# Kernel tuning notes

Measured on AMD Instinct MI355X. Metric: run time of the kernel, lower is better.

## Reference

```python
import jax, jax.numpy as jnp
import numpy as np

P = 16          # patch_size
C = 3           # in_chans
D = 768         # embed_dim
V = 10240       # position_embedding_size
B, H, W = 16, 512, 512
N = (H // P) * (W // P)  # 1024 patches per image


def setup_inputs() -> dict:
    key = jax.random.key(0)
    k1, k2, k3, k4, k5 = jax.random.split(key, 5)
    pixel_values = jax.random.uniform(k1, (B, C, H, W), dtype=jnp.float32)
    position_ids = jax.random.randint(k2, (B, N, 2), 0, 32)  # (x, y) patch coords < pW/pH
    padding_positions = jax.random.randint(k3, (B, N), 0, 2).astype(jnp.bool_)
    w_proj = jax.random.normal(k4, (D, C * P * P), dtype=jnp.float32) * 0.02  # Linear weight (out, in)
    pos_table = jax.random.normal(k5, (2, V, D), dtype=jnp.float32) * 0.02
    return {
        "pixel_values": pixel_values,
        "w_proj": w_proj,
        "pos_table": pos_table,
        "position_ids": position_ids,
        "padding_positions": padding_positions,
    }


def reference(pixel_values, w_proj, pos_table, position_ids, padding_positions):
    b, c, h, w = pixel_values.shape
    ph, pw = h // P, w // P
    # Extract patches in Gemma4 C-P-P flatten order: (B, N, C*P*P)
    x = pixel_values.reshape(b, c, ph, P, pw, P)
    x = jnp.transpose(x, (0, 2, 4, 1, 3, 5)).reshape(b, ph * pw, c * P * P)
    patches = 2.0 * (x - 0.5)
    hidden = jnp.einsum('bnf,df->bnd', patches, w_proj)
    # Position embeddings: one_hot(ids) @ table summed over the 2 axes
    # == direct gather-add: table[0][x_id] + table[1][y_id]
    ids = jnp.clip(position_ids, 0)
    pos = pos_table[0][ids[..., 0]] + pos_table[1][ids[..., 1]]  # (B, N, D)
    pos = jnp.where(padding_positions[..., None], 0.0, pos)
    return hidden + pos
```

## Files before the change

kernel.cpp:

```cpp
#include <hip/hip_runtime.h>
#include <stdint.h>


typedef __attribute__((ext_vector_type(8))) short bfrag_t;
typedef __attribute__((ext_vector_type(4))) float f4_t;
typedef __attribute__((ext_vector_type(8))) unsigned short u16x8;
typedef __attribute__((ext_vector_type(4))) unsigned short u16x4;

#define V_POS 10240

__device__ __forceinline__ unsigned short f2bf(float f) {
    unsigned int u = __float_as_uint(f);
    u += 0x7fffu + ((u >> 16) & 1u);
    return (unsigned short)(u >> 16);
}

__device__ __forceinline__ void async_ld16(const void* g, void* l) {
    __builtin_amdgcn_global_load_lds(
        (const __attribute__((address_space(1))) void*)g,
        (__attribute__((address_space(3))) void*)l, 16, 0, 0);
}

__global__ __launch_bounds__(256) void prep_kernel(
    const float* __restrict__ px, const float* __restrict__ wp,
    unsigned short* __restrict__ A, unsigned short* __restrict__ Wb)
{
    __shared__ unsigned short T[32 * 776];
    int bid = blockIdx.x, tid = threadIdx.x;
    if (bid < 512) {
        int b = bid >> 5, ph = bid & 31;
        const float* pxb = px + ((size_t)b * 3 * 512 + (size_t)ph * 16) * 512;
#pragma unroll 6
        for (int it = 0; it < 24; ++it) {
            int idx = it * 256 + tid;
            int c = idx >> 11, rem = idx & 2047, hl = rem >> 7, w4 = rem & 127;
            float4 v = *(const float4*)(pxb + (size_t)c * 262144 + hl * 512 + (w4 << 2));
            int pw  = w4 >> 2;
            int pxo = (w4 & 3) << 2;
            int k   = c * 256 + hl * 16 + pxo;
            u16x4 o;
            o[0] = f2bf(2.f * v.x - 1.f);
            o[1] = f2bf(2.f * v.y - 1.f);
            o[2] = f2bf(2.f * v.z - 1.f);
            o[3] = f2bf(2.f * v.w - 1.f);
            *(u16x4*)&T[pw * 776 + k] = o;
        }
        __syncthreads();
        int r = tid >> 3, p = tid & 7;
        unsigned short* Arow = A + ((size_t)bid * 32 + r) * 768;
        const unsigned short* Trow = T + r * 776;
#pragma unroll 4
        for (int j = 0; j < 12; ++j) {
            int co = (p + 8 * j) << 3;
            *(u16x8*)(Arow + co) = *(const u16x8*)(Trow + co);
        }
    } else {
        long idx = (long)(bid - 512) * 256 + tid;
        const float4* s = (const float4*)(wp + (idx << 3));
        float4 v0 = s[0], v1 = s[1];
        u16x8 o;
        o[0] = f2bf(v0.x); o[1] = f2bf(v0.y); o[2] = f2bf(v0.z); o[3] = f2bf(v0.w);
        o[4] = f2bf(v1.x); o[5] = f2bf(v1.y); o[6] = f2bf(v1.z); o[7] = f2bf(v1.w);
        *(u16x8*)(Wb + (idx << 3)) = o;
    }
}

__global__ __launch_bounds__(256, 3) void gemm_kernel(
    const unsigned short* __restrict__ A, const unsigned short* __restrict__ Bt,
    const int* __restrict__ pos_ids, const unsigned int* __restrict__ pad_in,
    const float* __restrict__ pos_table, float* __restrict__ out)
{
    __shared__ unsigned short LDS[3 * 8192];

    const int tid  = threadIdx.x;
    const int wave = tid >> 6;
    const int lane = tid & 63;

    const int id   = blockIdx.x;
    const int xcd  = id & 7;
    const int slot = id >> 3;
    const int bmg  = slot / 6;
    const int bm   = xcd * 16 + bmg;
    const int bn   = slot - bmg * 6;
    const int m0   = bm << 7;
    const int n0   = bn << 7;

    const bool u8mode = __any(pad_in[lane] > 1u);

    const int rl = lane >> 2;
    const int g  = (lane & 3) ^ (rl & 3);
    const unsigned short* aga0 = A  + (size_t)(m0 + wave * 32 + rl) * 768 + g * 8;
    const unsigned short* aga1 = aga0 + (size_t)16 * 768;
    const unsigned short* bga0 = Bt + (size_t)(n0 + wave * 32 + rl) * 768 + g * 8;
    const unsigned short* bga1 = bga0 + (size_t)16 * 768;
    const int l0 = wave * 32 * 32;
    const int l1 = l0 + 16 * 32;

    const int fr      = lane & 15;
    const int quad    = lane >> 4;
    const int row_off = (wave & 1) << 6;
    const int col_off = (wave >> 1) << 6;
    const int afro = (row_off + fr) * 32 + ((quad ^ (fr & 3)) << 3);
    const int bfro = (col_off + fr) * 32 + ((quad ^ (fr & 3)) << 3) + 4096;

    f4_t acc[4][4] = {};

    auto issue = [&](int t, int b) {
        unsigned short* Ab = (unsigned short*)LDS + b * 8192;
        unsigned short* Bb = Ab + 4096;
        const int ko = t * 32;
        async_ld16(aga0 + ko, Ab + l0);
        async_ld16(aga1 + ko, Ab + l1);
        async_ld16(bga0 + ko, Bb + l0);
        async_ld16(bga1 + ko, Bb + l1);
    };

    issue(0, 0);
    issue(1, 1);

    int bi = 0;
    for (int t = 0; t < 24; ++t) {
        if (t < 23) __builtin_amdgcn_s_waitcnt(0xF74);
        else        __builtin_amdgcn_s_waitcnt(0xF70);
        __builtin_amdgcn_sched_barrier(0);
        __builtin_amdgcn_s_barrier();
        __builtin_amdgcn_sched_barrier(0);
        if (t < 22) {
            int nb = bi + 2; if (nb >= 3) nb -= 3;
            issue(t + 2, nb);
        }
        const unsigned short* Ar = LDS + bi * 8192 + afro;
        const unsigned short* Br = LDS + bi * 8192 + bfro;
        bfrag_t a[4], b[4];
#pragma unroll
        for (int i = 0; i < 4; ++i) a[i] = *(const bfrag_t*)(Ar + i * 512);
#pragma unroll
        for (int i = 0; i < 4; ++i) b[i] = *(const bfrag_t*)(Br + i * 512);
#pragma unroll
        for (int mi = 0; mi < 4; ++mi)
#pragma unroll
            for (int ni = 0; ni < 4; ++ni)
                acc[mi][ni] = __builtin_amdgcn_mfma_f32_16x16x32_bf16(
                    a[mi], b[ni], acc[mi][ni], 0, 0, 0);
        if (++bi == 3) bi = 0;
    }

    const unsigned char* pad8 = (const unsigned char*)pad_in;
    const int colbase = n0 + col_off;
#pragma unroll
    for (int mi = 0; mi < 4; ++mi) {
#pragma unroll
        for (int reg = 0; reg < 4; ++reg) {
            int gm  = m0 + row_off + mi * 16 + (quad << 2) + reg;
            int xid = pos_ids[2 * gm];
            int yid = pos_ids[2 * gm + 1];
            xid = xid < 0 ? 0 : xid;
            yid = yid < 0 ? 0 : yid;
            bool p = u8mode ? (pad8[gm] != 0) : (pad_in[gm] != 0u);
            const float* t0 = pos_table + (size_t)xid * 768 + colbase;
            const float* t1 = pos_table + (size_t)(V_POS + yid) * 768 + colbase;
            float* orow = out + (size_t)gm * 768 + colbase;
#pragma unroll
            for (int ni = 0; ni < 4; ++ni) {
                int cc = ni * 16 + fr;
                float pos = p ? 0.f : (t0[cc] + t1[cc]);
                orow[cc] = acc[mi][ni][reg] + pos;
            }
        }
    }
}

extern "C" void kernel_launch(void* const* d_in, const int* in_sizes, int n_in,
                              void* d_out, int out_size, void* d_ws, size_t ws_size,
                              hipStream_t stream) {
    const float*        px  = (const float*)d_in[0];
    const float*        wp  = (const float*)d_in[1];
    const float*        pt  = (const float*)d_in[2];
    const int*          pid = (const int*)d_in[3];
    const unsigned int* pad = (const unsigned int*)d_in[4];

    unsigned short* A  = (unsigned short*)d_ws;
    unsigned short* Wb = A + (size_t)16384 * 768;

    prep_kernel<<<800, 256, 0, stream>>>(px, wp, A, Wb);
    gemm_kernel<<<768, 256, 0, stream>>>(A, Wb, pid, pad, pt, (float*)d_out);
}
```

Before: 179.2 us.

## Fuse patch extraction into GEMM and prepack weights into MFMA fragment layout

Removes the intermediate bf16 patch matrix. Each 512-thread block now loads two patch-rows of pixels directly into LDS and converts them to bf16 there, then computes a 64x768 output tile with 32x32x16 MFMAs. Weights are prepacked into a fragment-ordered layout so each wave reads them straight from global/L2 without staging in LDS. This cuts the global write and re-read of A and one kernel's worth of traffic. In exchange it drops the async multi-buffered pipeline, launches only 256 blocks, and relies on cache hits for the repeated weight reads.

```diff
diff --git a/kernel.cpp b/kernel.cpp
--- a/kernel.cpp
+++ b/kernel.cpp
@@ -3,11 +3,12 @@
 
 
 typedef __attribute__((ext_vector_type(8))) short bfrag_t;
-typedef __attribute__((ext_vector_type(4))) float f4_t;
+typedef __attribute__((ext_vector_type(16))) float f16acc;
 typedef __attribute__((ext_vector_type(8))) unsigned short u16x8;
 typedef __attribute__((ext_vector_type(4))) unsigned short u16x4;
 
 #define V_POS 10240
+#define RSA 776
 
 __device__ __forceinline__ unsigned short f2bf(float f) {
     unsigned int u = __float_as_uint(f);
@@ -15,156 +16,106 @@
     return (unsigned short)(u >> 16);
 }
 
-__device__ __forceinline__ void async_ld16(const void* g, void* l) {
-    __builtin_amdgcn_global_load_lds(
-        (const __attribute__((address_space(1))) void*)g,
-        (__attribute__((address_space(3))) void*)l, 16, 0, 0);
+__global__ __launch_bounds__(256) void bpack_kernel(
+    const float* __restrict__ wp, unsigned short* __restrict__ Bp)
+{
+    int u     = blockIdx.x * 256 + threadIdx.x;
+    int chunk = u >> 6;
+    int lane  = u & 63;
+    int n32   = chunk / 48;
+    int k16   = chunk - n32 * 48;
+    int n     = (n32 << 5) + (lane & 31);
+    int k     = (k16 << 4) + ((lane >> 5) << 3);
+    const float* s = wp + (size_t)n * 768 + k;
+    float4 v0 = *(const float4*)s;
+    float4 v1 = *(const float4*)(s + 4);
+    u16x8 o;
+    o[0] = f2bf(v0.x); o[1] = f2bf(v0.y); o[2] = f2bf(v0.z); o[3] = f2bf(v0.w);
+    o[4] = f2bf(v1.x); o[5] = f2bf(v1.y); o[6] = f2bf(v1.z); o[7] = f2bf(v1.w);
+    *(u16x8*)(Bp + (size_t)chunk * 512 + (lane << 3)) = o;
 }
 
-__global__ __launch_bounds__(256) void prep_kernel(
-    const float* __restrict__ px, const float* __restrict__ wp,
-    unsigned short* __restrict__ A, unsigned short* __restrict__ Wb)
-{
-    __shared__ unsigned short T[32 * 776];
-    int bid = blockIdx.x, tid = threadIdx.x;
-    if (bid < 512) {
-        int b = bid >> 5, ph = bid & 31;
-        const float* pxb = px + ((size_t)b * 3 * 512 + (size_t)ph * 16) * 512;
-#pragma unroll 6
-        for (int it = 0; it < 24; ++it) {
-            int idx = it * 256 + tid;
-            int c = idx >> 11, rem = idx & 2047, hl = rem >> 7, w4 = rem & 127;
-            float4 v = *(const float4*)(pxb + (size_t)c * 262144 + hl * 512 + (w4 << 2));
-            int pw  = w4 >> 2;
-            int pxo = (w4 & 3) << 2;
-            int k   = c * 256 + hl * 16 + pxo;
-            u16x4 o;
-            o[0] = f2bf(2.f * v.x - 1.f);
-            o[1] = f2bf(2.f * v.y - 1.f);
-            o[2] = f2bf(2.f * v.z - 1.f);
-            o[3] = f2bf(2.f * v.w - 1.f);
-            *(u16x4*)&T[pw * 776 + k] = o;
-        }
-        __syncthreads();
-        int r = tid >> 3, p = tid & 7;
-        unsigned short* Arow = A + ((size_t)bid * 32 + r) * 768;
-        const unsigned short* Trow = T + r * 776;
-#pragma unroll 4
-        for (int j = 0; j < 12; ++j) {
-            int co = (p + 8 * j) << 3;
-            *(u16x8*)(Arow + co) = *(const u16x8*)(Trow + co);
-        }
-    } else {
-        long idx = (long)(bid - 512) * 256 + tid;
-        const float4* s = (const float4*)(wp + (idx << 3));
-        float4 v0 = s[0], v1 = s[1];
-        u16x8 o;
-        o[0] = f2bf(v0.x); o[1] = f2bf(v0.y); o[2] = f2bf(v0.z); o[3] = f2bf(v0.w);
-        o[4] = f2bf(v1.x); o[5] = f2bf(v1.y); o[6] = f2bf(v1.z); o[7] = f2bf(v1.w);
-        *(u16x8*)(Wb + (idx << 3)) = o;
-    }
-}
-
-__global__ __launch_bounds__(256, 3) void gemm_kernel(
-    const unsigned short* __restrict__ A, const unsigned short* __restrict__ Bt,
+__global__ __launch_bounds__(512, 2) void fused_kernel(
+    const float* __restrict__ px, const unsigned short* __restrict__ Bp,
     const int* __restrict__ pos_ids, const unsigned int* __restrict__ pad_in,
     const float* __restrict__ pos_table, float* __restrict__ out)
 {
-    __shared__ unsigned short LDS[3 * 8192];
+    __shared__ unsigned short As[64 * RSA];
 
     const int tid  = threadIdx.x;
     const int wave = tid >> 6;
     const int lane = tid & 63;
+    const int bid  = blockIdx.x;
+    const int m0   = bid << 6;
+    const int img  = bid >> 4;
+    const int prow = bid & 15;
 
-    const int id   = blockIdx.x;
-    const int xcd  = id & 7;
-    const int slot = id >> 3;
-    const int bmg  = slot / 6;
-    const int bm   = xcd * 16 + bmg;
-    const int bn   = slot - bmg * 6;
-    const int m0   = bm << 7;
-    const int n0   = bn << 7;
+    const float* base = px + ((size_t)img * 3 * 512 + (size_t)prow * 32) * 512;
+#pragma unroll 6
+    for (int it = 0; it < 24; ++it) {
+        int idx = it * 512 + tid;
+        int c   = idx >> 12;
+        int rem = idx & 4095;
+        int hl  = rem >> 7;
+        int w4  = rem & 127;
+        float4 v = *(const float4*)(base + (size_t)c * 262144 + hl * 512 + (w4 << 2));
+        int r = ((hl >> 4) << 5) + (w4 >> 2);
+        int k = (c << 8) + ((hl & 15) << 4) + ((w4 & 3) << 2);
+        u16x4 o;
+        o[0] = f2bf(2.f * v.x - 1.f);
+        o[1] = f2bf(2.f * v.y - 1.f);
+        o[2] = f2bf(2.f * v.z - 1.f);
+        o[3] = f2bf(2.f * v.w - 1.f);
+        *(u16x4*)&As[r * RSA + k] = o;
+    }
+    __syncthreads();
 
     const bool u8mode = __any(pad_in[lane] > 1u);
 
-    const int rl = lane >> 2;
-    const int g  = (lane & 3) ^ (rl & 3);
-    const unsigned short* aga0 = A  + (size_t)(m0 + wave * 32 + rl) * 768 + g * 8;
-    const unsigned short* aga1 = aga0 + (size_t)16 * 768;
-    const unsigned short* bga0 = Bt + (size_t)(n0 + wave * 32 + rl) * 768 + g * 8;
-    const unsigned short* bga1 = bga0 + (size_t)16 * 768;
-    const int l0 = wave * 32 * 32;
-    const int l1 = l0 + 16 * 32;
+    const unsigned short* afrag = As + (size_t)(lane & 31) * RSA + ((lane >> 5) << 3);
+    const unsigned short* bbase = Bp + (size_t)(wave * 3) * 48 * 512 + (lane << 3);
 
-    const int fr      = lane & 15;
-    const int quad    = lane >> 4;
-    const int row_off = (wave & 1) << 6;
-    const int col_off = (wave >> 1) << 6;
-    const int afro = (row_off + fr) * 32 + ((quad ^ (fr & 3)) << 3);
-    const int bfro = (col_off + fr) * 32 + ((quad ^ (fr & 3)) << 3) + 4096;
+    f16acc acc[2][3] = {};
 
-    f4_t acc[4][4] = {};
-
-    auto issue = [&](int t, int b) {
-        unsigned short* Ab = (unsigned short*)LDS + b * 8192;
-        unsigned short* Bb = Ab + 4096;
-        const int ko = t * 32;
-        async_ld16(aga0 + ko, Ab + l0);
-        async_ld16(aga1 + ko, Ab + l1);
-        async_ld16(bga0 + ko, Bb + l0);
-        async_ld16(bga1 + ko, Bb + l1);
-    };
-
-    issue(0, 0);
-    issue(1, 1);
-
-    int bi = 0;
-    for (int t = 0; t < 24; ++t) {
-        if (t < 23) __builtin_amdgcn_s_waitcnt(0xF74);
-        else        __builtin_amdgcn_s_waitcnt(0xF70);
-        __builtin_amdgcn_sched_barrier(0);
-        __builtin_amdgcn_s_barrier();
-        __builtin_amdgcn_sched_barrier(0);
-        if (t < 22) {
-            int nb = bi + 2; if (nb >= 3) nb -= 3;
-            issue(t + 2, nb);
-        }
-        const unsigned short* Ar = LDS + bi * 8192 + afro;
-        const unsigned short* Br = LDS + bi * 8192 + bfro;
-        bfrag_t a[4], b[4];
-#pragma unroll
-        for (int i = 0; i < 4; ++i) a[i] = *(const bfrag_t*)(Ar + i * 512);
-#pragma unroll
-        for (int i = 0; i < 4; ++i) b[i] = *(const bfrag_t*)(Br + i * 512);
-#pragma unroll
-        for (int mi = 0; mi < 4; ++mi)
-#pragma unroll
-            for (int ni = 0; ni < 4; ++ni)
-                acc[mi][ni] = __builtin_amdgcn_mfma_f32_16x16x32_bf16(
-                    a[mi], b[ni], acc[mi][ni], 0, 0, 0);
-        if (++bi == 3) bi = 0;
+#pragma unroll 4
+    for (int k16 = 0; k16 < 48; ++k16) {
+        const unsigned short* ak = afrag + (k16 << 4);
+        bfrag_t a0 = *(const bfrag_t*)(ak);
+        bfrag_t a1 = *(const bfrag_t*)(ak + 32 * RSA);
+        const unsigned short* bk = bbase + (size_t)k16 * 512;
+        bfrag_t b0 = *(const bfrag_t*)(bk);
+        bfrag_t b1 = *(const bfrag_t*)(bk + 48 * 512);
+        bfrag_t b2 = *(const bfrag_t*)(bk + 96 * 512);
+        acc[0][0] = __builtin_amdgcn_mfma_f32_32x32x16_bf16(a0, b0, acc[0][0], 0, 0, 0);
+        acc[0][1] = __builtin_amdgcn_mfma_f32_32x32x16_bf16(a0, b1, acc[0][1], 0, 0, 0);
+        acc[0][2] = __builtin_amdgcn_mfma_f32_32x32x16_bf16(a0, b2, acc[0][2], 0, 0, 0);
+        acc[1][0] = __builtin_amdgcn_mfma_f32_32x32x16_bf16(a1, b0, acc[1][0], 0, 0, 0);
+        acc[1][1] = __builtin_amdgcn_mfma_f32_32x32x16_bf16(a1, b1, acc[1][1], 0, 0, 0);
+        acc[1][2] = __builtin_amdgcn_mfma_f32_32x32x16_bf16(a1, b2, acc[1][2], 0, 0, 0);
     }
 
     const unsigned char* pad8 = (const unsigned char*)pad_in;
-    const int colbase = n0 + col_off;
+    const int cl  = lane & 31;
+    const int h4  = (lane >> 5) << 2;
 #pragma unroll
-    for (int mi = 0; mi < 4; ++mi) {
+    for (int mt = 0; mt < 2; ++mt) {
 #pragma unroll
-        for (int reg = 0; reg < 4; ++reg) {
-            int gm  = m0 + row_off + mi * 16 + (quad << 2) + reg;
+        for (int r = 0; r < 16; ++r) {
+            int row = (mt << 5) + (r & 3) + ((r >> 2) << 3) + h4;
+            int gm  = m0 + row;
             int xid = pos_ids[2 * gm];
             int yid = pos_ids[2 * gm + 1];
             xid = xid < 0 ? 0 : xid;
             yid = yid < 0 ? 0 : yid;
             bool p = u8mode ? (pad8[gm] != 0) : (pad_in[gm] != 0u);
-            const float* t0 = pos_table + (size_t)xid * 768 + colbase;
-            const float* t1 = pos_table + (size_t)(V_POS + yid) * 768 + colbase;
-            float* orow = out + (size_t)gm * 768 + colbase;
+            const float* t0 = pos_table + (size_t)xid * 768;
+            const float* t1 = pos_table + (size_t)(V_POS + yid) * 768;
+            float* orow = out + (size_t)gm * 768;
 #pragma unroll
-            for (int ni = 0; ni < 4; ++ni) {
-                int cc = ni * 16 + fr;
-                float pos = p ? 0.f : (t0[cc] + t1[cc]);
-                orow[cc] = acc[mi][ni][reg] + pos;
+            for (int nt = 0; nt < 3; ++nt) {
+                int col = wave * 96 + (nt << 5) + cl;
+                float pos = p ? 0.f : (t0[col] + t1[col]);
+                orow[col] = acc[mt][nt][r] + pos;
             }
         }
     }
@@ -179,9 +130,8 @@
     const int*          pid = (const int*)d_in[3];
     const unsigned int* pad = (const unsigned int*)d_in[4];
 
-    unsigned short* A  = (unsigned short*)d_ws;
-    unsigned short* Wb = A + (size_t)16384 * 768;
+    unsigned short* Bp = (unsigned short*)d_ws;
 
-    prep_kernel<<<800, 256, 0, stream>>>(px, wp, A, Wb);
-    gemm_kernel<<<768, 256, 0, stream>>>(A, Wb, pid, pad, pt, (float*)d_out);
+    bpack_kernel<<<288, 256, 0, stream>>>(wp, Bp);
+    fused_kernel<<<256, 512, 0, stream>>>(px, Bp, pid, pad, pt, (float*)d_out);
 }
```

Result: faster. 174.0 us (-2.9%).
